# Optimization experiments

Measured on AMD Instinct MI355X. Metric: run time of the kernel, lower is better.

Reference implementation:

```python
import jax, jax.numpy as jnp
import numpy as np

N_NODES = 100000
N_EDGES = 1200000
EMBED_DIM = 64
CONV_DIMS = [64, 32, 16]
EPS = 1e-12


def setup_inputs() -> dict:
    key = jax.random.key(0)
    ks = jax.random.split(key, 16)
    def xavier(k, shape):
        fan_out, fan_in = shape
        bound = np.sqrt(6.0 / (fan_in + fan_out))
        return jax.random.uniform(k, shape, jnp.float32, -bound, bound)
    inp = {
        "entity_user_embed": jax.random.normal(ks[0], (N_NODES, EMBED_DIM), jnp.float32) * 0.1,
        "w1_0": xavier(ks[1], (64, 64)), "b1_0": jnp.zeros((64,), jnp.float32),
        "w2_0": xavier(ks[2], (64, 64)), "b2_0": jnp.zeros((64,), jnp.float32),
        "w1_1": xavier(ks[3], (32, 64)), "b1_1": jnp.zeros((32,), jnp.float32),
        "w2_1": xavier(ks[4], (32, 64)), "b2_1": jnp.zeros((32,), jnp.float32),
        "w1_2": xavier(ks[5], (16, 32)), "b1_2": jnp.zeros((16,), jnp.float32),
        "w2_2": xavier(ks[6], (16, 32)), "b2_2": jnp.zeros((16,), jnp.float32),
        "edge_val": jax.random.uniform(ks[7], (N_EDGES,), jnp.float32),
        "edge_row": jax.random.randint(ks[8], (N_EDGES,), 0, N_NODES, jnp.int32),
        "edge_col": jax.random.randint(ks[9], (N_EDGES,), 0, N_NODES, jnp.int32),
    }
    return inp


def _spmm(edge_val, edge_row, edge_col, x, n):
    # sparse A_in @ x : gather source rows, scale by edge value, scatter-add to dest
    msg = edge_val[:, None] * x[edge_col]          # [E, D]
    return jax.ops.segment_sum(msg, edge_row, num_segments=n)


def _aggregate(ego, side, w1, b1, w2, b2):
    # Aggregator: LeakyReLU(linear1(ego+side)) + LeakyReLU(linear2(ego*side))
    sum_e = jax.nn.leaky_relu((ego + side) @ w1.T + b1, negative_slope=0.01)
    bi_e = jax.nn.leaky_relu((ego * side) @ w2.T + b2, negative_slope=0.01)
    return sum_e + bi_e  # dropout is identity in eval mode


def _l2norm(x):
    n = jnp.sqrt(jnp.sum(x * x, axis=1, keepdims=True))
    return x / jnp.maximum(n, EPS)


def reference(entity_user_embed, w1_0, b1_0, w2_0, b2_0,
              w1_1, b1_1, w2_1, b2_1, w1_2, b1_2, w2_2, b2_2,
              edge_val, edge_row, edge_col):
    n = entity_user_embed.shape[0]
    layers = [(w1_0, b1_0, w2_0, b2_0), (w1_1, b1_1, w2_1, b2_1), (w1_2, b1_2, w2_2, b2_2)]
    ego = entity_user_embed
    all_embed = [ego]
    for (w1, b1, w2, b2) in layers:
        side = _spmm(edge_val, edge_row, edge_col, ego, n)
        ego = _aggregate(ego, side, w1, b1, w2, b2)
        all_embed.append(_l2norm(ego))
    return jnp.concatenate(all_embed, axis=1)  # [N, 64+64+32+16]
```

## Files before the change

kernel.cpp:

```cpp
#include <hip/hip_runtime.h>


#define NODES 100000
#define OUT_STRIDE 176

typedef _Float16 f16x8 __attribute__((ext_vector_type(8)));
typedef float f32x4 __attribute__((ext_vector_type(4)));
typedef _Float16 half4_t __attribute__((ext_vector_type(4)));
typedef unsigned long long u64;

static constexpr int NV = NODES + 1;
static constexpr int NB = 256;
static constexpr int BINH = (NODES + 255) / 256;
static constexpr int M_SCAN = BINH * NB;
static constexpr int NC1 = (M_SCAN + 1023) / 1024;
static constexpr int CAP = 4096;


__global__ __launch_bounds__(1024) void bucket_count_kernel(const int* __restrict__ rows,
                                                            int* __restrict__ gh,
                                                            int e, int chunk) {
    __shared__ int lh[BINH];
    for (int t = threadIdx.x; t < BINH; t += 1024) lh[t] = 0;
    __syncthreads();
    int b = blockIdx.x;
    int start = b * chunk, end = min(e, start + chunk);
    for (int i = start + threadIdx.x; i < end; i += 1024)
        atomicAdd(&lh[rows[i] >> 8], 1);
    __syncthreads();
    for (int t = threadIdx.x; t < BINH; t += 1024) gh[t * NB + b] = lh[t];
}

__global__ __launch_bounds__(1024) void scan_k1(const int* __restrict__ in, int* __restrict__ out,
                                                int* __restrict__ sums, int m) {
    int i = blockIdx.x * 1024 + threadIdx.x;
    int v = (i < m) ? in[i] : 0;
    int lane = threadIdx.x & 63, wid = threadIdx.x >> 6;
    int incl = v;
    #pragma unroll
    for (int off = 1; off < 64; off <<= 1) {
        int t = __shfl_up(incl, off);
        if (lane >= off) incl += t;
    }
    __shared__ int wsum[16];
    if (lane == 63) wsum[wid] = incl;
    __syncthreads();
    int woff = 0;
    for (int k = 0; k < wid; ++k) woff += wsum[k];
    if (i < m) out[i] = incl - v + woff;
    if (threadIdx.x == 1023) sums[blockIdx.x] = incl + woff;
}

__global__ __launch_bounds__(1024) void scan_k2(int* __restrict__ sums, int nc) {
    int t = threadIdx.x;
    int v = (t < nc) ? sums[t] : 0;
    int lane = t & 63, wid = t >> 6;
    int incl = v;
    #pragma unroll
    for (int off = 1; off < 64; off <<= 1) {
        int x = __shfl_up(incl, off);
        if (lane >= off) incl += x;
    }
    __shared__ int wsum[16];
    if (lane == 63) wsum[wid] = incl;
    __syncthreads();
    int woff = 0;
    for (int k = 0; k < wid; ++k) woff += wsum[k];
    if (t < nc) sums[t] = incl - v + woff;
}

__global__ __launch_bounds__(1024) void scan_k3(int* __restrict__ out, const int* __restrict__ sums,
                                                int m) {
    int i = blockIdx.x * 1024 + threadIdx.x;
    if (i < m) out[i] += sums[blockIdx.x];
}

__global__ __launch_bounds__(1024) void bucket_scatter_kernel(
    const int* __restrict__ rows, const int* __restrict__ cols, const float* __restrict__ vals,
    const int* __restrict__ ghs, u64* __restrict__ tmp, int e, int chunk) {
    __shared__ int cur[BINH];
    int b = blockIdx.x;
    for (int t = threadIdx.x; t < BINH; t += 1024) cur[t] = ghs[t * NB + b];
    __syncthreads();
    int start = b * chunk, end = min(e, start + chunk);
    for (int i = start + threadIdx.x; i < end; i += 1024) {
        int r = rows[i];
        unsigned v15 = __float2uint_rn(vals[i] * 32767.f);
        unsigned pk = (unsigned)cols[i] | (v15 << 17);
        int pos = atomicAdd(&cur[r >> 8], 1);
        tmp[pos] = ((u64)(unsigned)r << 32) | pk;
    }
}

__global__ __launch_bounds__(1024) void bucket_sort_kernel(
    const u64* __restrict__ tmp, const int* __restrict__ ghs,
    unsigned* __restrict__ sorted, int* __restrict__ row_ptr, int e) {
    __shared__ u64 ebuf[CAP];
    __shared__ int hist[256], bstart[256], cursor[256], ws4[4];
    int b = blockIdx.x, t = threadIdx.x;
    int base = ghs[b * NB];
    int endp = (b == BINH - 1) ? e : ghs[(b + 1) * NB];
    int size = min(endp - base, CAP);
    for (int i = t; i < 256; i += 1024) hist[i] = 0;
    __syncthreads();
    for (int i = t; i < size; i += 1024) {
        u64 ev = tmp[base + i];
        ebuf[i] = ev;
        atomicAdd(&hist[(int)(ev >> 32) & 255], 1);
    }
    __syncthreads();
    {
        int v = (t < 256) ? hist[t] : 0;
        int lane = t & 63, wid = t >> 6;
        int incl = v;
        #pragma unroll
        for (int off = 1; off < 64; off <<= 1) {
            int x = __shfl_up(incl, off);
            if (lane >= off) incl += x;
        }
        if (lane == 63 && wid < 4) ws4[wid] = incl;
        __syncthreads();
        if (t < 256) {
            int woff = 0;
            for (int k = 0; k < wid; ++k) woff += ws4[k];
            int ex = incl - v + woff;
            bstart[t] = ex;
            cursor[t] = ex;
            int rr = b * 256 + t;
            if (rr <= NODES) row_ptr[rr] = base + ex;
        }
    }
    __syncthreads();
    for (int i = t; i < size; i += 1024) {
        u64 ev = ebuf[i];
        int bin = (int)(ev >> 32) & 255;
        int pos = base + atomicAdd(&cursor[bin], 1);
        sorted[pos] = (unsigned)ev;
    }
}


__global__ void prep_embed_kernel(const float4* __restrict__ x4, float4* __restrict__ out4,
                                  half4_t* __restrict__ xh) {
    int i = blockIdx.x * blockDim.x + threadIdx.x;
    if (i < NODES * 16) {
        int r = i >> 4, c = i & 15;
        float4 v = x4[i];
        out4[r * (OUT_STRIDE / 4) + c] = v;
        xh[i] = half4_t{(_Float16)v.x, (_Float16)v.y, (_Float16)v.z, (_Float16)v.w};
    }
}


template <int DIN, int DOUT>
__global__ __launch_bounds__(256, 4) void layer_kernel(
    const _Float16* __restrict__ xh, const unsigned* __restrict__ edges,
    const int* __restrict__ row_ptr,
    const float* __restrict__ w1, const float* __restrict__ b1,
    const float* __restrict__ w2, const float* __restrict__ b2,
    _Float16* __restrict__ ego_out,
    float* __restrict__ outp,
    int n) {
    constexpr int KT = DIN / 32;
    constexpr int NT = DOUT / 16;
    constexpr int NFRAG = 2 * KT * NT;
    constexpr int DPL = DIN / 4;
    constexpr int C8 = DPL / 8;
    constexpr int SROWH = DIN + 8;

    __shared__ f16x8 wfrag[NFRAG * 64];
    __shared__ _Float16 tiles[4][2][16 * SROWH];

    for (int slot = threadIdx.x; slot < NFRAG * 64; slot += 256) {
        int l = slot & 63, fid = slot >> 6;
        int mat = fid / (KT * NT);
        int kt = (fid / NT) % KT;
        int nt = fid % NT;
        const float* w = mat ? w2 : w1;
        int o = nt * 16 + (l & 15);
        int kb = kt * 32 + (l >> 4) * 8;
        const float* src = w + o * DIN + kb;
        f16x8 f;
        #pragma unroll
        for (int jj = 0; jj < 8; ++jj) f[jj] = (_Float16)src[jj];
        wfrag[slot] = f;
    }
    __syncthreads();

    int wid = threadIdx.x >> 6, lane = threadIdx.x & 63;
    int g = lane >> 2, li = lane & 3;
    int q = lane >> 4, cl = lane & 15;

    float bias1[NT], bias2[NT];
    #pragma unroll
    for (int nt = 0; nt < NT; ++nt) {
        bias1[nt] = b1[nt * 16 + cl];
        bias2[nt] = b2[nt * 16 + cl];
    }

    int r0 = blockIdx.x * 64 + wid * 16;

    int r = r0 + g;
    bool valid = r < n;
    int rr = valid ? r : 0;
    int s = valid ? row_ptr[rr] : 0;
    int e = valid ? row_ptr[rr + 1] : 0;

    const _Float16* xrow = xh + (size_t)rr * DIN + li * DPL;
    f16x8 egoh[C8];
    #pragma unroll
    for (int c = 0; c < C8; ++c) egoh[c] = *(const f16x8*)(xrow + c * 8);

    float sd[DPL];
    #pragma unroll
    for (int d = 0; d < DPL; ++d) sd[d] = 0.f;

    const _Float16* xbase = xh + li * DPL;
    int j = s;
    for (; j + 3 < e; j += 4) {
        unsigned pk[4];
        #pragma unroll
        for (int k = 0; k < 4; ++k) pk[k] = edges[j + k];
        f16x8 xv[4][C8];
        #pragma unroll
        for (int k = 0; k < 4; ++k) {
            const _Float16* p = xbase + (size_t)(pk[k] & 0x1FFFFu) * DIN;
            #pragma unroll
            for (int c = 0; c < C8; ++c) xv[k][c] = *(const f16x8*)(p + c * 8);
        }
        #pragma unroll
        for (int k = 0; k < 4; ++k) {
            float vf = (float)(pk[k] >> 17);
            #pragma unroll
            for (int c = 0; c < C8; ++c)
                #pragma unroll
                for (int d = 0; d < 8; ++d)
                    sd[c * 8 + d] += vf * (float)xv[k][c][d];
        }
    }
    for (; j < e; ++j) {
        unsigned p = edges[j];
        float vf = (float)(p >> 17);
        const _Float16* xp = xbase + (size_t)(p & 0x1FFFFu) * DIN;
        #pragma unroll
        for (int c = 0; c < C8; ++c) {
            f16x8 xv = *(const f16x8*)(xp + c * 8);
            #pragma unroll
            for (int d = 0; d < 8; ++d) sd[c * 8 + d] += vf * (float)xv[d];
        }
    }

    _Float16* srow = &tiles[wid][0][g * SROWH + li * DPL];
    _Float16* brow = &tiles[wid][1][g * SROWH + li * DPL];
    constexpr float SCL = 1.f / 32767.f;
    #pragma unroll
    for (int c = 0; c < C8; ++c) {
        f16x8 sm, bi;
        #pragma unroll
        for (int d = 0; d < 8; ++d) {
            float egof = (float)egoh[c][d];
            float sv = sd[c * 8 + d] * SCL;
            sm[d] = (_Float16)(egof + sv);
            bi[d] = (_Float16)(egof * sv);
        }
        *(f16x8*)(srow + c * 8) = sm;
        *(f16x8*)(brow + c * 8) = bi;
    }

    f16x8 sumA[KT], biA[KT];
    #pragma unroll
    for (int kt = 0; kt < KT; ++kt) {
        sumA[kt] = *(const f16x8*)&tiles[wid][0][cl * SROWH + kt * 32 + q * 8];
        biA[kt]  = *(const f16x8*)&tiles[wid][1][cl * SROWH + kt * 32 + q * 8];
    }

    float ov[NT][4];
    #pragma unroll
    for (int nt = 0; nt < NT; ++nt) {
        f32x4 c1 = {bias1[nt], bias1[nt], bias1[nt], bias1[nt]};
        f32x4 c2 = {bias2[nt], bias2[nt], bias2[nt], bias2[nt]};
        #pragma unroll
        for (int kt = 0; kt < KT; ++kt) {
            f16x8 wa = wfrag[((0 * KT + kt) * NT + nt) * 64 + lane];
            f16x8 wb = wfrag[((1 * KT + kt) * NT + nt) * 64 + lane];
            c1 = __builtin_amdgcn_mfma_f32_16x16x32_f16(sumA[kt], wa, c1, 0, 0, 0);
            c2 = __builtin_amdgcn_mfma_f32_16x16x32_f16(biA[kt], wb, c2, 0, 0, 0);
        }
        #pragma unroll
        for (int t = 0; t < 4; ++t) {
            float u1 = c1[t] > 0.f ? c1[t] : 0.01f * c1[t];
            float u2 = c2[t] > 0.f ? c2[t] : 0.01f * c2[t];
            ov[nt][t] = u1 + u2;
        }
    }

    #pragma unroll
    for (int t = 0; t < 4; ++t) {
        float sq = 0.f;
        #pragma unroll
        for (int nt = 0; nt < NT; ++nt) sq += ov[nt][t] * ov[nt][t];
        #pragma unroll
        for (int off = 1; off < 16; off <<= 1) sq += __shfl_xor(sq, off);
        float inv = 1.f / fmaxf(sqrtf(sq), 1e-12f);
        int rw = r0 + 4 * q + t;
        if (rw < n) {
            #pragma unroll
            for (int nt = 0; nt < NT; ++nt) {
                float o = ov[nt][t];
                if (ego_out) ego_out[(size_t)rw * DOUT + nt * 16 + cl] = (_Float16)o;
                outp[(size_t)rw * OUT_STRIDE + nt * 16 + cl] = o * inv;
            }
        }
    }
}


static size_t align_up(size_t x) { return (x + 255) & ~(size_t)255; }

extern "C" void kernel_launch(void* const* d_in, const int* in_sizes, int n_in,
                              void* d_out, int out_size, void* d_ws, size_t ws_size,
                              hipStream_t stream) {
    const float* embed = (const float*)d_in[0];
    const float* w1_0 = (const float*)d_in[1];  const float* b1_0 = (const float*)d_in[2];
    const float* w2_0 = (const float*)d_in[3];  const float* b2_0 = (const float*)d_in[4];
    const float* w1_1 = (const float*)d_in[5];  const float* b1_1 = (const float*)d_in[6];
    const float* w2_1 = (const float*)d_in[7];  const float* b2_1 = (const float*)d_in[8];
    const float* w1_2 = (const float*)d_in[9];  const float* b1_2 = (const float*)d_in[10];
    const float* w2_2 = (const float*)d_in[11]; const float* b2_2 = (const float*)d_in[12];
    const float* edge_val = (const float*)d_in[13];
    const int*   edge_row = (const int*)d_in[14];
    const int*   edge_col = (const int*)d_in[15];
    const int E = in_sizes[14];
    const int N = in_sizes[0] / 64;
    float* out = (float*)d_out;

    char* ws = (char*)d_ws;
    size_t off = 0;
    int* row_ptr   = (int*)(ws + off); off = align_up(off + (size_t)NV * 4);
    int* gh        = (int*)(ws + off); off = align_up(off + (size_t)M_SCAN * 4);
    int* ghs       = (int*)(ws + off); off = align_up(off + (size_t)M_SCAN * 4);
    int* sums      = (int*)(ws + off); off = align_up(off + (size_t)256 * 4);
    u64* tmp       = (u64*)(ws + off); off = align_up(off + (size_t)E * 8);
    unsigned* sorted = (unsigned*)(ws + off); off = align_up(off + (size_t)E * 4);
    _Float16* embed_h = (_Float16*)(ws + off); off = align_up(off + (size_t)N * 64 * 2);
    _Float16* ego1_h  = (_Float16*)(ws + off); off = align_up(off + (size_t)N * 64 * 2);
    _Float16* ego2_h  = (_Float16*)(ws + off); off = align_up(off + (size_t)N * 32 * 2);
    (void)ws_size; (void)n_in; (void)out_size;

    int chunk = (E + NB - 1) / NB;
    bucket_count_kernel<<<NB, 1024, 0, stream>>>(edge_row, gh, E, chunk);
    scan_k1<<<NC1, 1024, 0, stream>>>(gh, ghs, sums, M_SCAN);
    scan_k2<<<1, 1024, 0, stream>>>(sums, NC1);
    scan_k3<<<NC1, 1024, 0, stream>>>(ghs, sums, M_SCAN);
    bucket_scatter_kernel<<<NB, 1024, 0, stream>>>(edge_row, edge_col, edge_val, ghs, tmp, E, chunk);
    bucket_sort_kernel<<<BINH, 1024, 0, stream>>>(tmp, ghs, sorted, row_ptr, E);

    prep_embed_kernel<<<(N * 16 + 255) / 256, 256, 0, stream>>>(
        (const float4*)embed, (float4*)out, (half4_t*)embed_h);

    int lb = (N + 63) / 64;
    layer_kernel<64, 64><<<lb, 256, 0, stream>>>(embed_h, sorted, row_ptr,
        w1_0, b1_0, w2_0, b2_0, ego1_h, out + 64, N);
    layer_kernel<64, 32><<<lb, 256, 0, stream>>>(ego1_h, sorted, row_ptr,
        w1_1, b1_1, w2_1, b2_1, ego2_h, out + 128, N);
    layer_kernel<32, 16><<<lb, 256, 0, stream>>>(ego2_h, sorted, row_ptr,
        w1_2, b1_2, w2_2, b2_2, nullptr, out + 160, N);
}
```

Baseline: 144.5 us.

## Accumulate SpMM gather in packed fp16 and enlarge layer blocks to 512 threads

The per-edge neighbour accumulation now runs in packed half-precision vectors instead of unpacked fp32 scalars. The edge-weight scale is folded into each weight before the multiply, which cuts conversion and FMA instruction count and register use. Layer blocks grow from 256 to 512 threads covering 128 rows, with launch bounds raised to 6 blocks per CU. The risk is lower accuracy from fp16 accumulation over about 12 edges per row, and more register pressure under the tighter occupancy target.

```diff
diff --git a/kernel.cpp b/kernel.cpp
--- a/kernel.cpp
+++ b/kernel.cpp
@@ -153,7 +153,7 @@
 
 
 template <int DIN, int DOUT>
-__global__ __launch_bounds__(256, 4) void layer_kernel(
+__global__ __launch_bounds__(512, 6) void layer_kernel(
     const _Float16* __restrict__ xh, const unsigned* __restrict__ edges,
     const int* __restrict__ row_ptr,
     const float* __restrict__ w1, const float* __restrict__ b1,
@@ -169,9 +169,9 @@
     constexpr int SROWH = DIN + 8;
 
     __shared__ f16x8 wfrag[NFRAG * 64];
-    __shared__ _Float16 tiles[4][2][16 * SROWH];
-
-    for (int slot = threadIdx.x; slot < NFRAG * 64; slot += 256) {
+    __shared__ _Float16 tiles[8][2][16 * SROWH];
+
+    for (int slot = threadIdx.x; slot < NFRAG * 64; slot += 512) {
         int l = slot & 63, fid = slot >> 6;
         int mat = fid / (KT * NT);
         int kt = (fid / NT) % KT;
@@ -198,7 +198,7 @@
         bias2[nt] = b2[nt * 16 + cl];
     }
 
-    int r0 = blockIdx.x * 64 + wid * 16;
+    int r0 = blockIdx.x * 128 + wid * 16;
 
     int r = r0 + g;
     bool valid = r < n;
@@ -211,10 +211,11 @@
     #pragma unroll
     for (int c = 0; c < C8; ++c) egoh[c] = *(const f16x8*)(xrow + c * 8);
 
-    float sd[DPL];
-    #pragma unroll
-    for (int d = 0; d < DPL; ++d) sd[d] = 0.f;
-
+    f16x8 accv[C8];
+    #pragma unroll
+    for (int c = 0; c < C8; ++c) accv[c] = (f16x8)(_Float16)0;
+
+    constexpr float SCL = 1.f / 32767.f;
     const _Float16* xbase = xh + li * DPL;
     int j = s;
     for (; j + 3 < e; j += 4) {
@@ -230,41 +231,27 @@
         }
         #pragma unroll
         for (int k = 0; k < 4; ++k) {
-            float vf = (float)(pk[k] >> 17);
+            _Float16 vh = (_Float16)((float)(pk[k] >> 17) * SCL);
             #pragma unroll
             for (int c = 0; c < C8; ++c)
-                #pragma unroll
-                for (int d = 0; d < 8; ++d)
-                    sd[c * 8 + d] += vf * (float)xv[k][c][d];
+                accv[c] += xv[k][c] * vh;
         }
     }
     for (; j < e; ++j) {
         unsigned p = edges[j];
-        float vf = (float)(p >> 17);
+        _Float16 vh = (_Float16)((float)(p >> 17) * SCL);
         const _Float16* xp = xbase + (size_t)(p & 0x1FFFFu) * DIN;
         #pragma unroll
-        for (int c = 0; c < C8; ++c) {
-            f16x8 xv = *(const f16x8*)(xp + c * 8);
-            #pragma unroll
-            for (int d = 0; d < 8; ++d) sd[c * 8 + d] += vf * (float)xv[d];
-        }
+        for (int c = 0; c < C8; ++c)
+            accv[c] += (*(const f16x8*)(xp + c * 8)) * vh;
     }
 
     _Float16* srow = &tiles[wid][0][g * SROWH + li * DPL];
     _Float16* brow = &tiles[wid][1][g * SROWH + li * DPL];
-    constexpr float SCL = 1.f / 32767.f;
     #pragma unroll
     for (int c = 0; c < C8; ++c) {
-        f16x8 sm, bi;
-        #pragma unroll
-        for (int d = 0; d < 8; ++d) {
-            float egof = (float)egoh[c][d];
-            float sv = sd[c * 8 + d] * SCL;
-            sm[d] = (_Float16)(egof + sv);
-            bi[d] = (_Float16)(egof * sv);
-        }
-        *(f16x8*)(srow + c * 8) = sm;
-        *(f16x8*)(brow + c * 8) = bi;
+        *(f16x8*)(srow + c * 8) = egoh[c] + accv[c];
+        *(f16x8*)(brow + c * 8) = egoh[c] * accv[c];
     }
 
     f16x8 sumA[KT], biA[KT];
@@ -358,11 +345,11 @@
     prep_embed_kernel<<<(N * 16 + 255) / 256, 256, 0, stream>>>(
         (const float4*)embed, (float4*)out, (half4_t*)embed_h);
 
-    int lb = (N + 63) / 64;
-    layer_kernel<64, 64><<<lb, 256, 0, stream>>>(embed_h, sorted, row_ptr,
+    int lb = (N + 127) / 128;
+    layer_kernel<64, 64><<<lb, 512, 0, stream>>>(embed_h, sorted, row_ptr,
         w1_0, b1_0, w2_0, b2_0, ego1_h, out + 64, N);
-    layer_kernel<64, 32><<<lb, 256, 0, stream>>>(ego1_h, sorted, row_ptr,
+    layer_kernel<64, 32><<<lb, 512, 0, stream>>>(ego1_h, sorted, row_ptr,
         w1_1, b1_1, w2_1, b2_1, ego2_h, out + 128, N);
-    layer_kernel<32, 16><<<lb, 256, 0, stream>>>(ego2_h, sorted, row_ptr,
+    layer_kernel<32, 16><<<lb, 512, 0, stream>>>(ego2_h, sorted, row_ptr,
         w1_2, b1_2, w2_2, b2_2, nullptr, out + 160, N);
 }
```

After: 133.5 us. 7.6% less time.
